# Kernel tuning notes

Measured on AMD Instinct MI355X. Metric: run time of the kernel, lower is better.

The kernel has to match this reference:

```python
import jax, jax.numpy as jnp
import numpy as np

E = 8      # N_experts (hard-coded in module)
K = 2      # top-k (hard-coded in module)


def setup_inputs() -> dict:
    key = jax.random.key(0)
    ks = jax.random.split(key, 8)
    B, T, d = 4, 2048, 1024
    h = 4 * d // E  # 512, per Expert hidden_dim = 4*d//N_experts
    s = 0.02
    X = jax.random.normal(ks[0], (B, T, d), jnp.float32)
    routing_W = jax.random.normal(ks[1], (E, d), jnp.float32) * s  # Linear(d,E,bias=False).weight
    expert_bias = jnp.zeros((E,), jnp.float32)
    sW1 = jax.random.normal(ks[2], (d, h), jnp.float32) * s
    sb1 = jnp.zeros((h,), jnp.float32)
    sW2 = jax.random.normal(ks[3], (h, d), jnp.float32) * s
    sb2 = jnp.zeros((d,), jnp.float32)
    rW1 = jax.random.normal(ks[4], (E, d, h), jnp.float32) * s
    rb1 = jnp.zeros((E, h), jnp.float32)
    rW2 = jax.random.normal(ks[5], (E, h, d), jnp.float32) * s
    rb2 = jnp.zeros((E, d), jnp.float32)
    return dict(X=X, routing_W=routing_W, expert_bias=expert_bias,
                sW1=sW1, sb1=sb1, sW2=sW2, sb2=sb2,
                rW1=rW1, rb1=rb1, rW2=rW2, rb2=rb2)


def reference(X, routing_W, expert_bias, sW1, sb1, sW2, sb2, rW1, rb1, rW2, rb2):
    B, T, d = X.shape
    # Shared expert MLP: Linear -> SiLU -> Linear
    shared = jax.nn.silu(X @ sW1 + sb1) @ sW2 + sb2  # [B,T,d]

    # Routing (layer_idx in {3,4,5} path): logits -> sqrt(softplus) -> top-2
    logits = jnp.einsum('btd,ed->bte', X, routing_W) + expert_bias  # [B,T,E]
    activation = jnp.sqrt(jax.nn.softplus(logits))
    top_vals, top_idx = jax.lax.top_k(activation, K)  # [B,T,K]

    # Per-token combine weights over experts: sum_k top_vals[k] * onehot(top_idx[k])
    combine = jnp.sum(jax.nn.one_hot(top_idx, E, dtype=X.dtype) * top_vals[..., None],
                      axis=-2)  # [B,T,E]

    # Dense all-expert compute (equivalent to masked gather + per-expert MLP +
    # scatter-add combine in the original; unrouted experts get weight 0).
    Xf = X.reshape(-1, d)          # [N,d], N = B*T
    cf = combine.reshape(-1, E)    # [N,E]
    hdn = jax.nn.silu(jnp.einsum('nd,edh->enh', Xf, rW1) + rb1[:, None, :])  # [E,N,h]
    y = jnp.einsum('enh,ehd->end', hdn, rW2) + rb2[:, None, :]               # [E,N,d]
    routed = jnp.einsum('ne,end->nd', cf, y).reshape(B, T, d)

    return shared + routed
```

## Files before the change

kernel.cpp:

```cpp
#include <hip/hip_runtime.h>
#include <hip/hip_bf16.h>
#include <stdint.h>

#define NTOK 8192
#define DDIM 1024
#define HDIM 512

typedef __attribute__((ext_vector_type(8))) __bf16 bf16x8;
typedef __attribute__((ext_vector_type(4))) float f32x4;
typedef __attribute__((ext_vector_type(4))) uint32_t u32x4;
typedef __attribute__((ext_vector_type(2))) uint32_t u32x2;

__device__ __forceinline__ void gload16(const void* g, void* lds) {
  __builtin_amdgcn_global_load_lds(
      (const __attribute__((address_space(1))) void*)g,
      (__attribute__((address_space(3))) void*)lds,
      16, 0, 0);
}


__global__ __launch_bounds__(256)
void convert_route_kernel(const float* __restrict__ X, const float* __restrict__ rW,
                          const float* __restrict__ ebias,
                          __hip_bfloat16* __restrict__ Xb,
                          int* __restrict__ top_e, float* __restrict__ top_w) {
  int wid = threadIdx.x >> 6, lane = threadIdx.x & 63;
  int tok = blockIdx.x * 4 + wid;
  const float4* xr = (const float4*)(X + (size_t)tok * DDIM);
  u32x2* xb = (u32x2*)(Xb + (size_t)tok * DDIM);
  float acc[8];
  #pragma unroll
  for (int e = 0; e < 8; e++) acc[e] = 0.f;
  #pragma unroll
  for (int c = 0; c < 4; c++) {
    int j = c * 64 + lane;
    float4 x = xr[j];
    union { __hip_bfloat16 h[4]; u32x2 u; } cv;
    cv.h[0] = __float2bfloat16(x.x); cv.h[1] = __float2bfloat16(x.y);
    cv.h[2] = __float2bfloat16(x.z); cv.h[3] = __float2bfloat16(x.w);
    xb[j] = cv.u;
    #pragma unroll
    for (int e = 0; e < 8; e++) {
      float4 w = ((const float4*)(rW + (size_t)e * DDIM))[j];
      acc[e] += x.x * w.x + x.y * w.y + x.z * w.z + x.w * w.w;
    }
  }
  #pragma unroll
  for (int m = 1; m < 64; m <<= 1)
    #pragma unroll
    for (int e = 0; e < 8; e++) acc[e] += __shfl_xor(acc[e], m, 64);
  if (lane == 0) {
    float act[8];
    #pragma unroll
    for (int e = 0; e < 8; e++) {
      float x = acc[e] + ebias[e];
      float sp = (x > 15.f) ? x : log1pf(expf(x));
      act[e] = sqrtf(sp);
    }
    int e1 = 0; float v1 = act[0];
    #pragma unroll
    for (int e = 1; e < 8; e++) if (act[e] > v1) { v1 = act[e]; e1 = e; }
    int e2 = -1; float v2 = -1.f;
    #pragma unroll
    for (int e = 0; e < 8; e++) if (e != e1 && act[e] > v2) { v2 = act[e]; e2 = e; }
    top_e[tok * 2] = e1; top_e[tok * 2 + 1] = e2;
    top_w[tok * 2] = v1; top_w[tok * 2 + 1] = v2;
  }
}

__global__ void convert_w_kernel(const float* __restrict__ sIn, const float* __restrict__ rIn,
                                 __hip_bfloat16* __restrict__ sOut, __hip_bfloat16* __restrict__ rOut,
                                 int K, int Nn) {
  __shared__ float tile[32][33];
  int z = blockIdx.z;
  const float* src = (z == 0) ? sIn : rIn + (size_t)(z - 1) * K * Nn;
  __hip_bfloat16* dst = (z == 0) ? sOut : rOut + (size_t)(z - 1) * K * Nn;
  int n0 = blockIdx.x * 32, k0 = blockIdx.y * 32;
  int c = threadIdx.x & 31, r = threadIdx.x >> 5;
  #pragma unroll
  for (int i = 0; i < 4; i++)
    tile[r + i * 8][c] = src[(size_t)(k0 + r + i * 8) * Nn + n0 + c];
  __syncthreads();
  #pragma unroll
  for (int i = 0; i < 4; i++)
    dst[(size_t)(n0 + r + i * 8) * K + k0 + c] = __float2bfloat16(tile[c][r + i * 8]);
}


__global__ void hist_kernel(const int* __restrict__ top_e, int* __restrict__ chunkHist) {
  __shared__ int h[8];
  if (threadIdx.x < 8) h[threadIdx.x] = 0;
  __syncthreads();
  int a = blockIdx.x * 256 + threadIdx.x;
  atomicAdd(&h[top_e[a]], 1);
  __syncthreads();
  if (threadIdx.x < 8) chunkHist[blockIdx.x * 8 + threadIdx.x] = h[threadIdx.x];
}

__global__ void scan_kernel(const int* __restrict__ chunkHist, int* __restrict__ chunkBase,
                            int* __restrict__ counts, int* __restrict__ offs,
                            int* __restrict__ tiles) {
  int e = threadIdx.x;
  if (e < 8) {
    int run = 0;
    for (int b = 0; b < 64; b++) { chunkBase[b * 8 + e] = run; run += chunkHist[b * 8 + e]; }
    counts[e] = run;
  }
  __syncthreads();
  if (e == 0) {
    int s = 0;
    for (int i = 0; i < 8; i++) { offs[i] = s; s += counts[i]; }
    offs[8] = s;
    int tb = 0;
    for (int i = 0; i < 8; i++) { tiles[i] = tb; tb += (counts[i] + 127) >> 7; }
    tiles[8] = tb;
  }
  __syncthreads();
  if (e < 8) {
    int base = offs[e];
    for (int b = 0; b < 64; b++) chunkBase[b * 8 + e] += base;
  }
}

__global__ void scatter_kernel(const int* __restrict__ top_e, const float* __restrict__ top_w,
                               const int* __restrict__ chunkBase,
                               int* __restrict__ list, float* __restrict__ wlist,
                               int* __restrict__ inv) {
  __shared__ int lcnt[8];
  if (threadIdx.x < 8) lcnt[threadIdx.x] = 0;
  __syncthreads();
  int a = blockIdx.x * 256 + threadIdx.x;
  int e = top_e[a];
  int p = atomicAdd(&lcnt[e], 1);
  int pos = chunkBase[blockIdx.x * 8 + e] + p;
  list[pos] = a >> 1;
  wlist[pos] = top_w[a];
  inv[a] = pos;
}


__global__ __launch_bounds__(256)
void combine_kernel(const int* __restrict__ inv, const __hip_bfloat16* __restrict__ ybuf,
                    float* __restrict__ out) {
  int tok = blockIdx.x;
  int c = threadIdx.x * 4;
  int p0 = inv[tok * 2], p1 = inv[tok * 2 + 1];
  size_t o = (size_t)tok * DDIM + c;
  float4 v = *(const float4*)(out + o);
  union { u32x2 u; __hip_bfloat16 h[4]; } y0, y1;
  y0.u = *(const u32x2*)(ybuf + (size_t)p0 * DDIM + c);
  y1.u = *(const u32x2*)(ybuf + (size_t)p1 * DDIM + c);
  v.x += __bfloat162float(y0.h[0]) + __bfloat162float(y1.h[0]);
  v.y += __bfloat162float(y0.h[1]) + __bfloat162float(y1.h[1]);
  v.z += __bfloat162float(y0.h[2]) + __bfloat162float(y1.h[2]);
  v.w += __bfloat162float(y0.h[3]) + __bfloat162float(y1.h[3]);
  *(float4*)(out + o) = v;
}


template<int MODE>
__global__ __launch_bounds__(256, 4)
void gemm_kernel(const __hip_bfloat16* __restrict__ Abase,
                 const __hip_bfloat16* __restrict__ Ws,
                 const __hip_bfloat16* __restrict__ Wr,
                 const float* __restrict__ bs,
                 const float* __restrict__ br,
                 __hip_bfloat16* __restrict__ Hout,
                 float* __restrict__ Oout,
                 __hip_bfloat16* __restrict__ Ybuf,
                 const int* __restrict__ counts,
                 const int* __restrict__ offs,
                 const int* __restrict__ tiles,
                 const int* __restrict__ list,
                 const float* __restrict__ wlist) {
  constexpr int K   = (MODE == 1) ? 1024 : 512;
  constexpr int NN  = (MODE == 1) ? 512 : 1024;
  constexpr int LDB = K * 2;
  constexpr int SH  = (MODE == 1) ? 256 : 512;
  constexpr int LNT = (MODE == 1) ? 2 : 3;

  __shared__ __hip_bfloat16 Abuf[128 * 32];
  __shared__ __hip_bfloat16 Bbuf[128 * 32];
  __shared__ int tokens[128];

  int l = ((blockIdx.x & 7) * (gridDim.x >> 3)) + (blockIdx.x >> 3);

  int e = 0, mt, nt;
  bool rb = false;
  if (l < SH) { mt = l >> LNT; nt = l & ((1 << LNT) - 1); }
  else {
    rb = true;
    int rq = l - SH;
    int rt = rq >> LNT; nt = rq & ((1 << LNT) - 1);
    if (rt >= tiles[8]) return;
    while (e < 7 && rt >= tiles[e + 1]) ++e;
    mt = rt - tiles[e];
  }
  int m0 = mt * 128;
  int cnt = 128;
  if (rb) {
    int ce = counts[e];
    cnt = (ce - m0 < 128) ? (ce - m0) : 128;
  }

  const __hip_bfloat16* W = rb ? (Wr + (size_t)e * NN * K) : Ws;
  const float* bias = rb ? (br + e * NN) : bs;

  int tid = threadIdx.x, wid = tid >> 6, lane = tid & 63;
  if (MODE == 1) {
    if (tid < 128)
      tokens[tid] = rb ? ((tid < cnt) ? list[offs[e] + m0 + tid] : 0) : (m0 + tid);
    __syncthreads();
  }
  int arow0 = rb ? (NTOK + offs[e] + m0) : m0;

  const char* aSrc[2];
  const char* bSrc[2];
  int ldsOff[2];
  #pragma unroll
  for (int c = 0; c < 2; c++) {
    int s = c * 4096 + wid * 1024 + lane * 16;
    int row = s >> 6;
    int chunk = (s >> 4) & 3;
    int sc = chunk ^ (row & 3);
    long ar = (MODE == 1) ? (long)tokens[row] : (long)(arow0 + row);
    aSrc[c] = (const char*)Abase + (size_t)ar * LDB + sc * 16;
    bSrc[c] = (const char*)W + (size_t)(nt * 128 + row) * LDB + sc * 16;
    ldsOff[c] = c * 4096 + wid * 1024;
  }

  int wm = wid >> 1, wn = wid & 1;
  int aoff[4], boff[4];
  #pragma unroll
  for (int m = 0; m < 4; m++) {
    int row = wm * 64 + m * 16 + (lane & 15);
    aoff[m] = row * 64 + (((lane >> 4) ^ (row & 3)) << 4);
  }
  #pragma unroll
  for (int n = 0; n < 4; n++) {
    int row = wn * 64 + n * 16 + (lane & 15);
    boff[n] = row * 64 + (((lane >> 4) ^ (row & 3)) << 4);
  }

  f32x4 zero = {0.f, 0.f, 0.f, 0.f};
  f32x4 acc[4][4];
  #pragma unroll
  for (int m = 0; m < 4; m++)
    #pragma unroll
    for (int n = 0; n < 4; n++) acc[m][n] = zero;

  char* ldsA = (char*)&Abuf[0];
  char* ldsB = (char*)&Bbuf[0];

  for (int kt = 0; kt < K / 32; ++kt) {
    __syncthreads();
    #pragma unroll
    for (int c = 0; c < 2; c++) gload16(aSrc[c] + (size_t)kt * 64, ldsA + ldsOff[c]);
    #pragma unroll
    for (int c = 0; c < 2; c++) gload16(bSrc[c] + (size_t)kt * 64, ldsB + ldsOff[c]);
    __syncthreads();
    bf16x8 a[4], b[4];
    #pragma unroll
    for (int m = 0; m < 4; m++) a[m] = *(const bf16x8*)(ldsA + aoff[m]);
    #pragma unroll
    for (int n = 0; n < 4; n++) b[n] = *(const bf16x8*)(ldsB + boff[n]);
    #pragma unroll
    for (int m = 0; m < 4; m++)
      #pragma unroll
      for (int n = 0; n < 4; n++)
        acc[m][n] = __builtin_amdgcn_mfma_f32_16x16x32_bf16(a[m], b[n], acc[m][n], 0, 0, 0);
  }

  int colBase = nt * 128 + wn * 64;
  if (MODE == 1) {
    size_t hrow0 = rb ? (size_t)(NTOK + offs[e] + m0) : (size_t)m0;
    #pragma unroll
    for (int m = 0; m < 4; m++) {
      #pragma unroll
      for (int r = 0; r < 4; r++) {
        int rl = wm * 64 + m * 16 + ((lane >> 4) << 2) + r;
        if (rl < cnt) {
          #pragma unroll
          for (int n = 0; n < 4; n++) {
            int col = colBase + n * 16 + (lane & 15);
            float v = acc[m][n][r] + bias[col];
            v = v / (1.f + __expf(-v));
            Hout[(hrow0 + rl) * HDIM + col] = __float2bfloat16(v);
          }
        }
      }
    }
  } else if (!rb) {
    #pragma unroll
    for (int m = 0; m < 4; m++) {
      #pragma unroll
      for (int r = 0; r < 4; r++) {
        int rl = wm * 64 + m * 16 + ((lane >> 4) << 2) + r;
        size_t orow = (size_t)(m0 + rl);
        #pragma unroll
        for (int n = 0; n < 4; n++) {
          int col = colBase + n * 16 + (lane & 15);
          Oout[orow * DDIM + col] = acc[m][n][r] + bias[col];
        }
      }
    }
  } else {
    #pragma unroll
    for (int m = 0; m < 4; m++) {
      #pragma unroll
      for (int r = 0; r < 4; r++) {
        int rl = wm * 64 + m * 16 + ((lane >> 4) << 2) + r;
        if (rl < cnt) {
          int pos = offs[e] + m0 + rl;
          float w = wlist[pos];
          #pragma unroll
          for (int n = 0; n < 4; n++) {
            int col = colBase + n * 16 + (lane & 15);
            Ybuf[(size_t)pos * DDIM + col] = __float2bfloat16(w * (acc[m][n][r] + bias[col]));
          }
        }
      }
    }
  }
}


extern "C" void kernel_launch(void* const* d_in, const int* in_sizes, int n_in,
                              void* d_out, int out_size, void* d_ws, size_t ws_size,
                              hipStream_t stream) {
  const float* X   = (const float*)d_in[0];
  const float* rWt = (const float*)d_in[1];
  const float* eb  = (const float*)d_in[2];
  const float* sW1 = (const float*)d_in[3];
  const float* sb1 = (const float*)d_in[4];
  const float* sW2 = (const float*)d_in[5];
  const float* sb2 = (const float*)d_in[6];
  const float* rW1 = (const float*)d_in[7];
  const float* rb1 = (const float*)d_in[8];
  const float* rW2 = (const float*)d_in[9];
  const float* rb2 = (const float*)d_in[10];
  float* out = (float*)d_out;

  char* ws = (char*)d_ws;
  size_t off = 0;
  auto alloc = [&](size_t bytes) {
    char* p = ws + off;
    off += (bytes + 255) & ~(size_t)255;
    return p;
  };
  char* region0 = alloc((size_t)16384 * DDIM * 2);
  __hip_bfloat16* Xb   = (__hip_bfloat16*)region0;
  __hip_bfloat16* sW1t = (__hip_bfloat16*)(region0 + (size_t)NTOK * DDIM * 2);
  __hip_bfloat16* rW1t = (__hip_bfloat16*)(region0 + (size_t)NTOK * DDIM * 2
                                                   + (size_t)HDIM * DDIM * 2);
  __hip_bfloat16* Ybuf = (__hip_bfloat16*)region0;

  __hip_bfloat16* sW2t = (__hip_bfloat16*)alloc((size_t)DDIM * HDIM * 2);
  __hip_bfloat16* rW2t = (__hip_bfloat16*)alloc((size_t)8 * DDIM * HDIM * 2);
  __hip_bfloat16* Hbuf = (__hip_bfloat16*)alloc((size_t)(NTOK + 2 * NTOK) * HDIM * 2);
  alloc(131072);
  int* counts    = (int*)alloc(64);
  int* offsA     = (int*)alloc(64);
  int* tiles     = (int*)alloc(64);
  int* top_e     = (int*)alloc((size_t)NTOK * 2 * 4);
  float* top_w   = (float*)alloc((size_t)NTOK * 2 * 4);
  int* list      = (int*)alloc((size_t)NTOK * 2 * 4);
  float* wlist   = (float*)alloc((size_t)NTOK * 2 * 4);
  int* inv       = (int*)alloc((size_t)NTOK * 2 * 4);
  int* chunkHist = (int*)alloc(64 * 8 * 4);
  int* chunkBase = (int*)alloc(64 * 8 * 4);

  convert_route_kernel<<<2048, 256, 0, stream>>>(X, rWt, eb, Xb, top_e, top_w);
  convert_w_kernel<<<dim3(16, 32, 9), 256, 0, stream>>>(sW1, rW1, sW1t, rW1t, 1024, 512);
  convert_w_kernel<<<dim3(32, 16, 9), 256, 0, stream>>>(sW2, rW2, sW2t, rW2t, 512, 1024);
  hist_kernel<<<64, 256, 0, stream>>>(top_e, chunkHist);
  scan_kernel<<<1, 64, 0, stream>>>(chunkHist, chunkBase, counts, offsA, tiles);
  scatter_kernel<<<64, 256, 0, stream>>>(top_e, top_w, chunkBase, list, wlist, inv);
  gemm_kernel<1><<<256 + 4 * 136, 256, 0, stream>>>(Xb, sW1t, rW1t, sb1, rb1, Hbuf, out,
                                                    nullptr, counts, offsA, tiles, list, wlist);
  gemm_kernel<23><<<512 + 8 * 136, 256, 0, stream>>>(Hbuf, sW2t, rW2t, sb2, rb2, nullptr, out,
                                                     Ybuf, counts, offsA, tiles, list, wlist);
  combine_kernel<<<NTOK, 256, 0, stream>>>(inv, Ybuf, out);
}
```

Before: 264.1 us.

## Double-buffer GEMM LDS, fuse combine into shared GEMM2, merge hist and scan

The GEMM main loop now uses two LDS buffers, so the next K-tile's global-to-LDS load is issued while the current tile feeds the MFMAs, with one barrier per iteration instead of two. The LDS row swizzle is also changed. The second GEMM is split into a routed launch (MODE 3) that writes weighted Ybuf rows, followed by a shared launch (MODE 2) whose epilogue adds the two routed rows through inv, which removes the separate combine kernel and its extra pass over out. The histogram and scan kernels are merged into one single-block kernel, trading parallel atomics for serial counting loops and saving one launch.

Measured after the change: 270.6 us. +2.5%, slower.

```diff
diff --git a/kernel.cpp b/kernel.cpp
--- a/kernel.cpp
+++ b/kernel.cpp
@@ -8,7 +8,6 @@
 
 typedef __attribute__((ext_vector_type(8))) __bf16 bf16x8;
 typedef __attribute__((ext_vector_type(4))) float f32x4;
-typedef __attribute__((ext_vector_type(4))) uint32_t u32x4;
 typedef __attribute__((ext_vector_type(2))) uint32_t u32x2;
 
 __device__ __forceinline__ void gload16(const void* g, void* lds) {
@@ -87,39 +86,38 @@
 }
 
 
-__global__ void hist_kernel(const int* __restrict__ top_e, int* __restrict__ chunkHist) {
-  __shared__ int h[8];
-  if (threadIdx.x < 8) h[threadIdx.x] = 0;
-  __syncthreads();
-  int a = blockIdx.x * 256 + threadIdx.x;
-  atomicAdd(&h[top_e[a]], 1);
-  __syncthreads();
-  if (threadIdx.x < 8) chunkHist[blockIdx.x * 8 + threadIdx.x] = h[threadIdx.x];
-}
-
-__global__ void scan_kernel(const int* __restrict__ chunkHist, int* __restrict__ chunkBase,
-                            int* __restrict__ counts, int* __restrict__ offs,
-                            int* __restrict__ tiles) {
-  int e = threadIdx.x;
-  if (e < 8) {
+__global__ __launch_bounds__(512)
+void hist_scan_kernel(const int* __restrict__ top_e, int* __restrict__ chunkBase,
+                      int* __restrict__ counts, int* __restrict__ offs,
+                      int* __restrict__ tiles) {
+  __shared__ int hist[64][8];
+  __shared__ int cnt_s[8];
+  __shared__ int offs_s[8];
+  int i = threadIdx.x;
+  int c = i >> 3, e = i & 7;
+  const int* p = top_e + c * 256;
+  int n = 0;
+  for (int j = 0; j < 256; j++) n += (p[j] == e) ? 1 : 0;
+  hist[c][e] = n;
+  __syncthreads();
+  if (i < 8) {
     int run = 0;
-    for (int b = 0; b < 64; b++) { chunkBase[b * 8 + e] = run; run += chunkHist[b * 8 + e]; }
-    counts[e] = run;
-  }
-  __syncthreads();
-  if (e == 0) {
-    int s = 0;
-    for (int i = 0; i < 8; i++) { offs[i] = s; s += counts[i]; }
+    for (int b = 0; b < 64; b++) { int t = hist[b][i]; hist[b][i] = run; run += t; }
+    cnt_s[i] = run;
+    counts[i] = run;
+  }
+  __syncthreads();
+  if (i == 0) {
+    int s = 0, tb = 0;
+    for (int k = 0; k < 8; k++) {
+      offs_s[k] = s; offs[k] = s; s += cnt_s[k];
+      tiles[k] = tb; tb += (cnt_s[k] + 127) >> 7;
+    }
     offs[8] = s;
-    int tb = 0;
-    for (int i = 0; i < 8; i++) { tiles[i] = tb; tb += (counts[i] + 127) >> 7; }
     tiles[8] = tb;
   }
   __syncthreads();
-  if (e < 8) {
-    int base = offs[e];
-    for (int b = 0; b < 64; b++) chunkBase[b * 8 + e] += base;
-  }
+  chunkBase[c * 8 + e] = hist[c][e] + offs_s[e];
 }
 
 __global__ void scatter_kernel(const int* __restrict__ top_e, const float* __restrict__ top_w,
@@ -136,25 +134,6 @@
   list[pos] = a >> 1;
   wlist[pos] = top_w[a];
   inv[a] = pos;
-}
-
-
-__global__ __launch_bounds__(256)
-void combine_kernel(const int* __restrict__ inv, const __hip_bfloat16* __restrict__ ybuf,
-                    float* __restrict__ out) {
-  int tok = blockIdx.x;
-  int c = threadIdx.x * 4;
-  int p0 = inv[tok * 2], p1 = inv[tok * 2 + 1];
-  size_t o = (size_t)tok * DDIM + c;
-  float4 v = *(const float4*)(out + o);
-  union { u32x2 u; __hip_bfloat16 h[4]; } y0, y1;
-  y0.u = *(const u32x2*)(ybuf + (size_t)p0 * DDIM + c);
-  y1.u = *(const u32x2*)(ybuf + (size_t)p1 * DDIM + c);
-  v.x += __bfloat162float(y0.h[0]) + __bfloat162float(y1.h[0]);
-  v.y += __bfloat162float(y0.h[1]) + __bfloat162float(y1.h[1]);
-  v.z += __bfloat162float(y0.h[2]) + __bfloat162float(y1.h[2]);
-  v.w += __bfloat162float(y0.h[3]) + __bfloat162float(y1.h[3]);
-  *(float4*)(out + o) = v;
 }
 
 
@@ -172,25 +151,27 @@
                  const int* __restrict__ offs,
                  const int* __restrict__ tiles,
                  const int* __restrict__ list,
-                 const float* __restrict__ wlist) {
-  constexpr int K   = (MODE == 1) ? 1024 : 512;
-  constexpr int NN  = (MODE == 1) ? 512 : 1024;
-  constexpr int LDB = K * 2;
-  constexpr int SH  = (MODE == 1) ? 256 : 512;
-  constexpr int LNT = (MODE == 1) ? 2 : 3;
-
-  __shared__ __hip_bfloat16 Abuf[128 * 32];
-  __shared__ __hip_bfloat16 Bbuf[128 * 32];
+                 const float* __restrict__ wlist,
+                 const int* __restrict__ inv) {
+  constexpr int K    = (MODE == 1) ? 1024 : 512;
+  constexpr int NN   = (MODE == 1) ? 512 : 1024;
+  constexpr int LDBy = K * 2;
+  constexpr int LNT  = (MODE == 1) ? 2 : 3;
+  constexpr int NT   = K / 32;
+
+  __shared__ __hip_bfloat16 Abuf[2][128 * 32];
+  __shared__ __hip_bfloat16 Bbuf[2][128 * 32];
   __shared__ int tokens[128];
 
   int l = ((blockIdx.x & 7) * (gridDim.x >> 3)) + (blockIdx.x >> 3);
 
   int e = 0, mt, nt;
   bool rb = false;
-  if (l < SH) { mt = l >> LNT; nt = l & ((1 << LNT) - 1); }
+  if (MODE == 2) { mt = l >> 3; nt = l & 7; }
+  else if (MODE == 1 && l < 256) { mt = l >> 2; nt = l & 3; }
   else {
     rb = true;
-    int rq = l - SH;
+    int rq = (MODE == 1) ? (l - 256) : l;
     int rt = rq >> LNT; nt = rq & ((1 << LNT) - 1);
     if (rt >= tiles[8]) return;
     while (e < 7 && rt >= tiles[e + 1]) ++e;
@@ -219,14 +200,15 @@
   int ldsOff[2];
   #pragma unroll
   for (int c = 0; c < 2; c++) {
-    int s = c * 4096 + wid * 1024 + lane * 16;
-    int row = s >> 6;
-    int chunk = (s >> 4) & 3;
-    int sc = chunk ^ (row & 3);
-    long ar = (MODE == 1) ? (long)tokens[row] : (long)(arow0 + row);
-    aSrc[c] = (const char*)Abase + (size_t)ar * LDB + sc * 16;
-    bSrc[c] = (const char*)W + (size_t)(nt * 128 + row) * LDB + sc * 16;
     ldsOff[c] = c * 4096 + wid * 1024;
+    int s = ldsOff[c] + lane * 16;
+    int rho = s >> 6;
+    int klin = (s >> 4) & 3;
+    int r = rho ^ ((rho >> 2) & 1);
+    int k = klin ^ (r & 3);
+    long ar = (MODE == 1) ? (long)tokens[r] : (long)(arow0 + r);
+    aSrc[c] = (const char*)Abase + (size_t)ar * LDBy + k * 16;
+    bSrc[c] = (const char*)W + (size_t)(nt * 128 + r) * LDBy + k * 16;
   }
 
   int wm = wid >> 1, wn = wid & 1;
@@ -234,12 +216,16 @@
   #pragma unroll
   for (int m = 0; m < 4; m++) {
     int row = wm * 64 + m * 16 + (lane & 15);
-    aoff[m] = row * 64 + (((lane >> 4) ^ (row & 3)) << 4);
+    int rr = row ^ ((row >> 2) & 1);
+    int kk = (lane >> 4) ^ (row & 3);
+    aoff[m] = rr * 64 + kk * 16;
   }
   #pragma unroll
   for (int n = 0; n < 4; n++) {
     int row = wn * 64 + n * 16 + (lane & 15);
-    boff[n] = row * 64 + (((lane >> 4) ^ (row & 3)) << 4);
+    int rr = row ^ ((row >> 2) & 1);
+    int kk = (lane >> 4) ^ (row & 3);
+    boff[n] = rr * 64 + kk * 16;
   }
 
   f32x4 zero = {0.f, 0.f, 0.f, 0.f};
@@ -249,26 +235,34 @@
     #pragma unroll
     for (int n = 0; n < 4; n++) acc[m][n] = zero;
 
-  char* ldsA = (char*)&Abuf[0];
-  char* ldsB = (char*)&Bbuf[0];
-
-  for (int kt = 0; kt < K / 32; ++kt) {
-    __syncthreads();
-    #pragma unroll
-    for (int c = 0; c < 2; c++) gload16(aSrc[c] + (size_t)kt * 64, ldsA + ldsOff[c]);
-    #pragma unroll
-    for (int c = 0; c < 2; c++) gload16(bSrc[c] + (size_t)kt * 64, ldsB + ldsOff[c]);
-    __syncthreads();
+  auto stage = [&](int buf, int kt) {
+    #pragma unroll
+    for (int c = 0; c < 2; c++)
+      gload16(aSrc[c] + (size_t)kt * 64, (char*)&Abuf[0][0] + buf * 8192 + ldsOff[c]);
+    #pragma unroll
+    for (int c = 0; c < 2; c++)
+      gload16(bSrc[c] + (size_t)kt * 64, (char*)&Bbuf[0][0] + buf * 8192 + ldsOff[c]);
+  };
+
+  stage(0, 0);
+  __syncthreads();
+  int cur = 0;
+  for (int kt = 0; kt < NT; ++kt) {
+    if (kt + 1 < NT) stage(cur ^ 1, kt + 1);
+    const char* lA = (const char*)&Abuf[0][0] + cur * 8192;
+    const char* lB = (const char*)&Bbuf[0][0] + cur * 8192;
     bf16x8 a[4], b[4];
     #pragma unroll
-    for (int m = 0; m < 4; m++) a[m] = *(const bf16x8*)(ldsA + aoff[m]);
-    #pragma unroll
-    for (int n = 0; n < 4; n++) b[n] = *(const bf16x8*)(ldsB + boff[n]);
+    for (int m = 0; m < 4; m++) a[m] = *(const bf16x8*)(lA + aoff[m]);
+    #pragma unroll
+    for (int n = 0; n < 4; n++) b[n] = *(const bf16x8*)(lB + boff[n]);
     #pragma unroll
     for (int m = 0; m < 4; m++)
       #pragma unroll
       for (int n = 0; n < 4; n++)
         acc[m][n] = __builtin_amdgcn_mfma_f32_16x16x32_bf16(a[m], b[n], acc[m][n], 0, 0, 0);
+    __syncthreads();
+    cur ^= 1;
   }
 
   int colBase = nt * 128 + wn * 64;
@@ -290,17 +284,21 @@
         }
       }
     }
-  } else if (!rb) {
+  } else if (MODE == 2) {
     #pragma unroll
     for (int m = 0; m < 4; m++) {
       #pragma unroll
       for (int r = 0; r < 4; r++) {
         int rl = wm * 64 + m * 16 + ((lane >> 4) << 2) + r;
-        size_t orow = (size_t)(m0 + rl);
+        int t = m0 + rl;
+        int p0 = inv[t * 2], p1 = inv[t * 2 + 1];
         #pragma unroll
         for (int n = 0; n < 4; n++) {
           int col = colBase + n * 16 + (lane & 15);
-          Oout[orow * DDIM + col] = acc[m][n][r] + bias[col];
+          float v = acc[m][n][r] + bias[col]
+                  + __bfloat162float(Ybuf[(size_t)p0 * DDIM + col])
+                  + __bfloat162float(Ybuf[(size_t)p1 * DDIM + col]);
+          Oout[(size_t)t * DDIM + col] = v;
         }
       }
     }
@@ -367,18 +365,17 @@
   int* list      = (int*)alloc((size_t)NTOK * 2 * 4);
   float* wlist   = (float*)alloc((size_t)NTOK * 2 * 4);
   int* inv       = (int*)alloc((size_t)NTOK * 2 * 4);
-  int* chunkHist = (int*)alloc(64 * 8 * 4);
   int* chunkBase = (int*)alloc(64 * 8 * 4);
 
   convert_route_kernel<<<2048, 256, 0, stream>>>(X, rWt, eb, Xb, top_e, top_w);
   convert_w_kernel<<<dim3(16, 32, 9), 256, 0, stream>>>(sW1, rW1, sW1t, rW1t, 1024, 512);
   convert_w_kernel<<<dim3(32, 16, 9), 256, 0, stream>>>(sW2, rW2, sW2t, rW2t, 512, 1024);
-  hist_kernel<<<64, 256, 0, stream>>>(top_e, chunkHist);
-  scan_kernel<<<1, 64, 0, stream>>>(chunkHist, chunkBase, counts, offsA, tiles);
+  hist_scan_kernel<<<1, 512, 0, stream>>>(top_e, chunkBase, counts, offsA, tiles);
   scatter_kernel<<<64, 256, 0, stream>>>(top_e, top_w, chunkBase, list, wlist, inv);
   gemm_kernel<1><<<256 + 4 * 136, 256, 0, stream>>>(Xb, sW1t, rW1t, sb1, rb1, Hbuf, out,
-                                                    nullptr, counts, offsA, tiles, list, wlist);
-  gemm_kernel<23><<<512 + 8 * 136, 256, 0, stream>>>(Hbuf, sW2t, rW2t, sb2, rb2, nullptr, out,
-                                                     Ybuf, counts, offsA, tiles, list, wlist);
-  combine_kernel<<<NTOK, 256, 0, stream>>>(inv, Ybuf, out);
-}
+                                                    nullptr, counts, offsA, tiles, list, wlist, inv);
+  gemm_kernel<3><<<8 * 136, 256, 0, stream>>>(Hbuf, sW2t, rW2t, sb2, rb2, nullptr, out,
+                                              Ybuf, counts, offsA, tiles, list, wlist, inv);
+  gemm_kernel<2><<<64 * 8, 256, 0, stream>>>(Hbuf, sW2t, rW2t, sb2, rb2, nullptr, out,
+                                             Ybuf, counts, offsA, tiles, list, wlist, inv);
+}
```
